# Kernel tuning notes

Hardware: AMD Instinct MI355X
Metric: run time of the kernel (lower is better)

The kernel has to match this reference:

```python
import jax, jax.numpy as jnp
import numpy as np

# ---- config constants (from ResidualNetConfig) ----
BOUND_LO = jnp.array([-5.0, -5.0, -5.0], dtype=jnp.float32)
BOUND_DIS = jnp.array([10.0, 10.0, 10.0], dtype=jnp.float32)
N_MIN = 200                 # int(ceil(max extent)/resolution) = 10/0.05
PER_LEVEL_SCALE = 2.0
NUM_LEVELS = 4
LOG2_T = 19
T = 1 << LOG2_T
OUTPUT_SDF_SCALE = 0.1
LEAKY_SLOPE = 0.01

# Instant-NGP spatial hash primes (first coord uses 1)
PRIMES = (np.uint32(1), np.uint32(2654435761), np.uint32(805459861))
# 8 corner offsets of the unit cube, [8, 3]
CORNERS = jnp.array([[(c >> d) & 1 for d in range(3)] for c in range(8)], dtype=jnp.uint32)


def hash_grid_encode(xyz01, tables):
    """xyz01: [N,3] in [0,1]; tables: [L,T,F] -> [N, L*F] trilinear hashed features."""
    feats = []
    for l in range(NUM_LEVELS):
        res = jnp.float32(N_MIN * (PER_LEVEL_SCALE ** l))
        pos = xyz01 * res                       # [N,3]
        pfloor = jnp.floor(pos)
        frac = pos - pfloor                     # [N,3]
        base = pfloor.astype(jnp.uint32)        # [N,3]
        corner = base[:, None, :] + CORNERS[None, :, :]   # [N,8,3]
        h = (corner[..., 0] * PRIMES[0]) ^ (corner[..., 1] * PRIMES[1]) ^ (corner[..., 2] * PRIMES[2])
        idx = (h & jnp.uint32(T - 1)).astype(jnp.int32)   # [N,8]
        f = tables[l][idx]                      # [N,8,F] irregular gather
        # trilinear weights: prod over dims of frac (corner=1) or 1-frac (corner=0)
        w = jnp.prod(jnp.where(CORNERS[None].astype(bool), frac[:, None, :], 1.0 - frac[:, None, :]), axis=-1)  # [N,8]
        feats.append(jnp.sum(f * w[..., None], axis=1))   # [N,F]
    return jnp.concatenate(feats, axis=-1)      # [N, L*F]


def leaky_relu(x):
    return jnp.where(x >= 0, x, LEAKY_SLOPE * x)


def setup_inputs() -> dict:
    key = jax.random.key(0)
    k1, k2, k3, k4, k5 = jax.random.split(key, 5)
    N = 2_000_000
    xyz = jax.random.uniform(k1, (N, 3), dtype=jnp.float32) * BOUND_DIS + BOUND_LO
    tables = jax.random.normal(k2, (NUM_LEVELS, T, 2), dtype=jnp.float32) * 1e-2
    W_in = jax.random.normal(k3, (8, 64), dtype=jnp.float32) / np.sqrt(8.0)
    W_h = jax.random.normal(k4, (64, 64), dtype=jnp.float32) / np.sqrt(64.0)
    W_out = jax.random.normal(k5, (64, 1), dtype=jnp.float32) / np.sqrt(64.0)
    return {"xyz": xyz, "tables": tables, "W_in": W_in, "W_h": W_h, "W_out": W_out}


def reference(xyz, tables, W_in, W_h, W_out):
    # scale_with_bound: map xyz into [0,1]^3
    xyz01 = (xyz - BOUND_LO) / BOUND_DIS
    enc = hash_grid_encode(xyz01, tables)        # [N, 8]
    h = leaky_relu(enc @ W_in)                   # hidden layer 1
    h = leaky_relu(h @ W_h)                      # hidden layer 2
    sdf = (h @ W_out).reshape(-1) * OUTPUT_SDF_SCALE
    return sdf
```

## Files before the change

kernel.cpp:

```cpp
#include <hip/hip_runtime.h>
#include <hip/hip_fp16.h>

static constexpr unsigned TSIZE = 1u << 19;
static constexpr unsigned TMASK = TSIZE - 1u;

typedef _Float16 f16;
typedef f16   f16x8 __attribute__((ext_vector_type(8)));
typedef float f32x4 __attribute__((ext_vector_type(4)));

union H2U { __half2 h; unsigned u; };

__global__ __launch_bounds__(256)
void cvt_tables(const float4* __restrict__ in, __half2* __restrict__ out, int n4)
{
    int i = blockIdx.x * 256 + threadIdx.x;
    if (i < n4) {
        float4 v = in[i];
        out[2 * i]     = __floats2half2_rn(v.x, v.y);
        out[2 * i + 1] = __floats2half2_rn(v.z, v.w);
    }
}

__device__ __forceinline__ void hash_level(float px, float py, float pz, int l,
                                           const __half2* __restrict__ tab,
                                           float& e0, float& e1)
{
    const float res = 200.0f * (float)(1 << l);
    const float fx = px * res, fy = py * res, fz = pz * res;
    const float flx = floorf(fx), fly = floorf(fy), flz = floorf(fz);
    const float frx = fx - flx, fry = fy - fly, frz = fz - flz;
    const unsigned bx = (unsigned)flx, by = (unsigned)fly, bz = (unsigned)flz;
    const unsigned hy0 = by * 2654435761u, hy1 = (by + 1u) * 2654435761u;
    const unsigned hz0 = bz * 805459861u,  hz1 = (bz + 1u) * 805459861u;
    const float wx[2] = {1.0f - frx, frx};
    const float wy[2] = {1.0f - fry, fry};
    const float wz[2] = {1.0f - frz, frz};
    e0 = 0.0f; e1 = 0.0f;
    #pragma unroll
    for (int c = 0; c < 8; ++c) {
        unsigned h = (bx + (unsigned)(c & 1))
                   ^ ((c & 2) ? hy1 : hy0)
                   ^ ((c & 4) ? hz1 : hz0);
        __half2 fv = tab[h & TMASK];
        float2 f = __half22float2(fv);
        float w = wx[c & 1] * wy[(c >> 1) & 1] * wz[(c >> 2) & 1];
        e0 = fmaf(f.x, w, e0);
        e1 = fmaf(f.y, w, e1);
    }
}

__device__ __forceinline__ void stage_xyz(const float* __restrict__ xyz, int bbase, int N,
                                          float* sxyz, float& px, float& py, float& pz)
{
    const int g3 = bbase * 3;
    #pragma unroll
    for (int t = 0; t < 3; ++t) {
        int sidx = (int)threadIdx.x + t * 256;
        int g = g3 + sidx;
        sxyz[sidx] = (g < 3 * N) ? __builtin_nontemporal_load(&xyz[g]) : 0.0f;
    }
    __syncthreads();
    px = (sxyz[threadIdx.x * 3 + 0] + 5.0f) * 0.1f;
    py = (sxyz[threadIdx.x * 3 + 1] + 5.0f) * 0.1f;
    pz = (sxyz[threadIdx.x * 3 + 2] + 5.0f) * 0.1f;
}

__global__ __launch_bounds__(256, 8)
void encode01(const float* __restrict__ xyz, const __half2* __restrict__ tab16,
              unsigned long long* __restrict__ enc01, int N)
{
    __shared__ float sxyz[768];
    const int bbase = blockIdx.x * 256;
    const int i = bbase + (int)threadIdx.x;
    float px, py, pz;
    stage_xyz(xyz, bbase, N, sxyz, px, py, pz);

    float e0, e1, e2, e3;
    hash_level(px, py, pz, 0, tab16,         e0, e1);
    hash_level(px, py, pz, 1, tab16 + TSIZE, e2, e3);

    H2U a, b;
    a.h = __floats2half2_rn(e0, e1);
    b.h = __floats2half2_rn(e2, e3);
    if (i < N) {
        unsigned long long v = (unsigned long long)a.u
                             | ((unsigned long long)b.u << 32);
        __builtin_nontemporal_store(v, &enc01[i]);
    }
}

static constexpr int H1_STRIDE = 72;

__global__ __launch_bounds__(256, 2)
void mlp23_mfma(const float* __restrict__ xyz, const __half2* __restrict__ tab16,
                const unsigned long long* __restrict__ enc01,
                const float* __restrict__ Win, const float* __restrict__ Wh,
                const float* __restrict__ Wout, float* __restrict__ out, int N)
{
    __shared__ float sxyz[768];
    __shared__ f16 h1s[256 * H1_STRIDE];

    const int bbase = blockIdx.x * 256;
    const int i = bbase + (int)threadIdx.x;
    float px, py, pz;
    stage_xyz(xyz, bbase, N, sxyz, px, py, pz);

    float enc[8];
    {
        unsigned long long v = __builtin_nontemporal_load(&enc01[i < N ? i : 0]);
        H2U a, b; a.u = (unsigned)v; b.u = (unsigned)(v >> 32);
        float2 f01 = __half22float2(a.h);
        float2 f23 = __half22float2(b.h);
        enc[0] = f01.x; enc[1] = f01.y; enc[2] = f23.x; enc[3] = f23.y;
    }
    hash_level(px, py, pz, 2, tab16 + 2 * TSIZE, enc[4], enc[5]);
    hash_level(px, py, pz, 3, tab16 + 3 * TSIZE, enc[6], enc[7]);

    float h1[64];
    #pragma unroll
    for (int j = 0; j < 64; ++j) h1[j] = 0.0f;
    #pragma unroll
    for (int k = 0; k < 8; ++k) {
        const float e = enc[k];
        #pragma unroll
        for (int j = 0; j < 64; ++j)
            h1[j] = fmaf(e, Win[k * 64 + j], h1[j]);
    }
    {
        f16* row = &h1s[(int)threadIdx.x * H1_STRIDE];
        #pragma unroll
        for (int jj = 0; jj < 8; ++jj) {
            f16x8 v;
            #pragma unroll
            for (int e = 0; e < 8; ++e) {
                float a = h1[jj * 8 + e];
                a = (a >= 0.0f) ? a : 0.01f * a;
                v[e] = (f16)a;
            }
            *(f16x8*)(row + jj * 8) = v;
        }
    }
    __syncthreads();

    const int wave = (int)threadIdx.x >> 6;
    const int lane = (int)threadIdx.x & 63;
    const int c = lane & 15;
    const int q = lane >> 4;
    const f16* wbase = &h1s[wave * 64 * H1_STRIDE];

    f16x8 bfrag[2][4];
    #pragma unroll
    for (int kt = 0; kt < 2; ++kt)
        #pragma unroll
        for (int nt = 0; nt < 4; ++nt)
            #pragma unroll
            for (int j = 0; j < 8; ++j)
                bfrag[kt][nt][j] = (f16)Wh[(kt * 32 + q * 8 + j) * 64 + nt * 16 + c];

    f32x4 Ct[4][4];
    #pragma unroll
    for (int mt = 0; mt < 4; ++mt)
        #pragma unroll
        for (int nt = 0; nt < 4; ++nt)
            Ct[mt][nt] = (f32x4){0.f, 0.f, 0.f, 0.f};

    #pragma unroll
    for (int mt = 0; mt < 4; ++mt) {
        #pragma unroll
        for (int kt = 0; kt < 2; ++kt) {
            const f16x8 a = *(const f16x8*)&wbase[(mt * 16 + c) * H1_STRIDE + kt * 32 + q * 8];
            #pragma unroll
            for (int nt = 0; nt < 4; ++nt)
                Ct[mt][nt] = __builtin_amdgcn_mfma_f32_16x16x32_f16(a, bfrag[kt][nt], Ct[mt][nt], 0, 0, 0);
        }
    }

    float acc3[4][4];
    #pragma unroll
    for (int mt = 0; mt < 4; ++mt)
        #pragma unroll
        for (int r = 0; r < 4; ++r) acc3[mt][r] = 0.0f;

    #pragma unroll
    for (int nt = 0; nt < 4; ++nt) {
        const float wo = Wout[nt * 16 + c];
        #pragma unroll
        for (int mt = 0; mt < 4; ++mt)
            #pragma unroll
            for (int r = 0; r < 4; ++r) {
                float v = Ct[mt][nt][r];
                v = (v >= 0.0f) ? v : 0.01f * v;
                acc3[mt][r] = fmaf(v, wo, acc3[mt][r]);
            }
    }
    #pragma unroll
    for (int mask = 1; mask <= 8; mask <<= 1)
        #pragma unroll
        for (int mt = 0; mt < 4; ++mt)
            #pragma unroll
            for (int r = 0; r < 4; ++r)
                acc3[mt][r] += __shfl_xor(acc3[mt][r], mask, 64);

    if (c == 0) {
        #pragma unroll
        for (int mt = 0; mt < 4; ++mt)
            #pragma unroll
            for (int r = 0; r < 4; ++r) {
                int p = bbase + wave * 64 + mt * 16 + q * 4 + r;
                if (p < N) out[p] = acc3[mt][r] * 0.1f;
            }
    }
}

__global__ __launch_bounds__(256, 2)
void resnet_mono(const float* __restrict__ xyz, const float* __restrict__ tables,
                 const float* __restrict__ Win, const float* __restrict__ Wh,
                 const float* __restrict__ Wout, float* __restrict__ out, int N)
{
    __shared__ float sxyz[768];
    const int bbase = blockIdx.x * 256;
    const int i = bbase + (int)threadIdx.x;
    float px, py, pz;
    stage_xyz(xyz, bbase, N, sxyz, px, py, pz);

    float enc[8];
    #pragma unroll
    for (int l = 0; l < 4; ++l) {
        const float res = 200.0f * (float)(1 << l);
        const float fx = px * res, fy = py * res, fz = pz * res;
        const float flx = floorf(fx), fly = floorf(fy), flz = floorf(fz);
        const float frx = fx - flx, fry = fy - fly, frz = fz - flz;
        const unsigned bx = (unsigned)flx, by = (unsigned)fly, bz = (unsigned)flz;
        const unsigned hy0 = by * 2654435761u, hy1 = (by + 1u) * 2654435761u;
        const unsigned hz0 = bz * 805459861u,  hz1 = (bz + 1u) * 805459861u;
        const float wx[2] = {1.0f - frx, frx};
        const float wy[2] = {1.0f - fry, fry};
        const float wz[2] = {1.0f - frz, frz};
        const float2* tab = (const float2*)tables + (size_t)l * TSIZE;
        float e0 = 0.0f, e1 = 0.0f;
        #pragma unroll
        for (int cc = 0; cc < 8; ++cc) {
            unsigned h = (bx + (unsigned)(cc & 1))
                       ^ ((cc & 2) ? hy1 : hy0)
                       ^ ((cc & 4) ? hz1 : hz0);
            float2 f = tab[h & TMASK];
            float w = wx[cc & 1] * wy[(cc >> 1) & 1] * wz[(cc >> 2) & 1];
            e0 = fmaf(f.x, w, e0);
            e1 = fmaf(f.y, w, e1);
        }
        enc[2 * l] = e0; enc[2 * l + 1] = e1;
    }

    float h1[64];
    #pragma unroll
    for (int j = 0; j < 64; ++j) h1[j] = 0.0f;
    #pragma unroll
    for (int k = 0; k < 8; ++k) {
        const float e = enc[k];
        #pragma unroll
        for (int j = 0; j < 64; ++j)
            h1[j] = fmaf(e, Win[k * 64 + j], h1[j]);
    }
    #pragma unroll
    for (int j = 0; j < 64; ++j)
        h1[j] = (h1[j] >= 0.0f) ? h1[j] : 0.01f * h1[j];

    float sdf = 0.0f;
    #pragma unroll
    for (int j0 = 0; j0 < 64; j0 += 16) {
        float acc[16];
        #pragma unroll
        for (int jj = 0; jj < 16; ++jj) acc[jj] = 0.0f;
        #pragma unroll
        for (int k = 0; k < 64; ++k) {
            const float hk = h1[k];
            #pragma unroll
            for (int jj = 0; jj < 16; ++jj)
                acc[jj] = fmaf(hk, Wh[k * 64 + j0 + jj], acc[jj]);
        }
        #pragma unroll
        for (int jj = 0; jj < 16; ++jj) {
            float a = acc[jj];
            a = (a >= 0.0f) ? a : 0.01f * a;
            sdf = fmaf(a, Wout[j0 + jj], sdf);
        }
    }
    if (i < N) out[i] = sdf * 0.1f;
}

extern "C" void kernel_launch(void* const* d_in, const int* in_sizes, int n_in,
                              void* d_out, int out_size, void* d_ws, size_t ws_size,
                              hipStream_t stream) {
    const float* xyz    = (const float*)d_in[0];
    const float* tables = (const float*)d_in[1];
    const float* Win    = (const float*)d_in[2];
    const float* Wh     = (const float*)d_in[3];
    const float* Wout   = (const float*)d_in[4];
    float* out = (float*)d_out;

    const int N = in_sizes[0] / 3;
    const int blocks = (N + 255) / 256;

    const int tab_floats = in_sizes[1];
    const size_t tab16_bytes = (size_t)tab_floats * 2;
    const size_t enc01_bytes = (size_t)N * 8;

    if (ws_size >= tab16_bytes + enc01_bytes) {
        __half2* tab16 = (__half2*)d_ws;
        unsigned long long* enc01 = (unsigned long long*)((char*)d_ws + tab16_bytes);
        int n4 = tab_floats / 4;
        hipLaunchKernelGGL(cvt_tables, dim3((n4 + 255) / 256), dim3(256), 0, stream,
                           (const float4*)tables, tab16, n4);
        hipLaunchKernelGGL(encode01, dim3(blocks), dim3(256), 0, stream,
                           xyz, tab16, enc01, N);
        hipLaunchKernelGGL(mlp23_mfma, dim3(blocks), dim3(256), 0, stream,
                           xyz, tab16, enc01, Win, Wh, Wout, out, N);
    } else {
        hipLaunchKernelGGL(resnet_mono, dim3(blocks), dim3(256), 0, stream,
                           xyz, tables, Win, Wh, Wout, out, N);
    }
}
```

Before: 324.9 us.

## Fuse level 0-1 encoding into MFMA MLP kernel and pre-transpose Wh to fp16

Merges the separate encode01 kernel into the main MFMA kernel, which now computes all four hash levels itself. This removes the intermediate enc01 buffer write and read and one launch, at the cost of more gather latency inside a kernel limited to 2 blocks per SM. A tiny kernel now pre-transposes and converts Wh to fp16 so each thread loads its B fragments as single vector loads instead of strided scalar float loads. The earlier split may have been chosen to give the gathers higher occupancy, which the fused kernel gives up.

```diff
diff --git a/kernel.cpp b/kernel.cpp
--- a/kernel.cpp
+++ b/kernel.cpp
@@ -7,8 +7,6 @@
 typedef _Float16 f16;
 typedef f16   f16x8 __attribute__((ext_vector_type(8)));
 typedef float f32x4 __attribute__((ext_vector_type(4)));
-
-union H2U { __half2 h; unsigned u; };
 
 __global__ __launch_bounds__(256)
 void cvt_tables(const float4* __restrict__ in, __half2* __restrict__ out, int n4)
@@ -18,6 +16,18 @@
         float4 v = in[i];
         out[2 * i]     = __floats2half2_rn(v.x, v.y);
         out[2 * i + 1] = __floats2half2_rn(v.z, v.w);
+    }
+}
+
+__global__ __launch_bounds__(256)
+void cvt_wht(const float* __restrict__ Wh, f16* __restrict__ wht)
+{
+    int t = threadIdx.x;
+    #pragma unroll
+    for (int e = 0; e < 16; ++e) {
+        int idx = t * 16 + e;
+        int n = idx >> 6, k = idx & 63;
+        wht[n * 64 + k] = (f16)Wh[k * 64 + n];
     }
 }
 
@@ -49,70 +59,37 @@
     }
 }
 
-__device__ __forceinline__ void stage_xyz(const float* __restrict__ xyz, int bbase, int N,
-                                          float* sxyz, float& px, float& py, float& pz)
-{
-    const int g3 = bbase * 3;
-    #pragma unroll
-    for (int t = 0; t < 3; ++t) {
-        int sidx = (int)threadIdx.x + t * 256;
-        int g = g3 + sidx;
-        sxyz[sidx] = (g < 3 * N) ? __builtin_nontemporal_load(&xyz[g]) : 0.0f;
-    }
-    __syncthreads();
-    px = (sxyz[threadIdx.x * 3 + 0] + 5.0f) * 0.1f;
-    py = (sxyz[threadIdx.x * 3 + 1] + 5.0f) * 0.1f;
-    pz = (sxyz[threadIdx.x * 3 + 2] + 5.0f) * 0.1f;
-}
-
-__global__ __launch_bounds__(256, 8)
-void encode01(const float* __restrict__ xyz, const __half2* __restrict__ tab16,
-              unsigned long long* __restrict__ enc01, int N)
+static constexpr int H1_STRIDE = 72;
+
+__global__ __launch_bounds__(256, 2)
+void resnet_mfma(const float* __restrict__ xyz, const __half2* __restrict__ tab16,
+                 const f16* __restrict__ wht,
+                 const float* __restrict__ Win,
+                 const float* __restrict__ Wout, float* __restrict__ out, int N)
 {
     __shared__ float sxyz[768];
+    __shared__ f16 h1s[256 * H1_STRIDE];
+
     const int bbase = blockIdx.x * 256;
     const int i = bbase + (int)threadIdx.x;
-    float px, py, pz;
-    stage_xyz(xyz, bbase, N, sxyz, px, py, pz);
-
-    float e0, e1, e2, e3;
-    hash_level(px, py, pz, 0, tab16,         e0, e1);
-    hash_level(px, py, pz, 1, tab16 + TSIZE, e2, e3);
-
-    H2U a, b;
-    a.h = __floats2half2_rn(e0, e1);
-    b.h = __floats2half2_rn(e2, e3);
-    if (i < N) {
-        unsigned long long v = (unsigned long long)a.u
-                             | ((unsigned long long)b.u << 32);
-        __builtin_nontemporal_store(v, &enc01[i]);
-    }
-}
-
-static constexpr int H1_STRIDE = 72;
-
-__global__ __launch_bounds__(256, 2)
-void mlp23_mfma(const float* __restrict__ xyz, const __half2* __restrict__ tab16,
-                const unsigned long long* __restrict__ enc01,
-                const float* __restrict__ Win, const float* __restrict__ Wh,
-                const float* __restrict__ Wout, float* __restrict__ out, int N)
-{
-    __shared__ float sxyz[768];
-    __shared__ f16 h1s[256 * H1_STRIDE];
-
-    const int bbase = blockIdx.x * 256;
-    const int i = bbase + (int)threadIdx.x;
-    float px, py, pz;
-    stage_xyz(xyz, bbase, N, sxyz, px, py, pz);
+
+    {
+        const int g3 = bbase * 3;
+        #pragma unroll
+        for (int t = 0; t < 3; ++t) {
+            int sidx = (int)threadIdx.x + t * 256;
+            int g = g3 + sidx;
+            sxyz[sidx] = (g < 3 * N) ? __builtin_nontemporal_load(&xyz[g]) : 0.0f;
+        }
+    }
+    __syncthreads();
+    const float px = (sxyz[threadIdx.x * 3 + 0] + 5.0f) * 0.1f;
+    const float py = (sxyz[threadIdx.x * 3 + 1] + 5.0f) * 0.1f;
+    const float pz = (sxyz[threadIdx.x * 3 + 2] + 5.0f) * 0.1f;
 
     float enc[8];
-    {
-        unsigned long long v = __builtin_nontemporal_load(&enc01[i < N ? i : 0]);
-        H2U a, b; a.u = (unsigned)v; b.u = (unsigned)(v >> 32);
-        float2 f01 = __half22float2(a.h);
-        float2 f23 = __half22float2(b.h);
-        enc[0] = f01.x; enc[1] = f01.y; enc[2] = f23.x; enc[3] = f23.y;
-    }
+    hash_level(px, py, pz, 0, tab16,             enc[0], enc[1]);
+    hash_level(px, py, pz, 1, tab16 + TSIZE,     enc[2], enc[3]);
     hash_level(px, py, pz, 2, tab16 + 2 * TSIZE, enc[4], enc[5]);
     hash_level(px, py, pz, 3, tab16 + 3 * TSIZE, enc[6], enc[7]);
 
@@ -153,9 +130,7 @@
     for (int kt = 0; kt < 2; ++kt)
         #pragma unroll
         for (int nt = 0; nt < 4; ++nt)
-            #pragma unroll
-            for (int j = 0; j < 8; ++j)
-                bfrag[kt][nt][j] = (f16)Wh[(kt * 32 + q * 8 + j) * 64 + nt * 16 + c];
+            bfrag[kt][nt] = *(const f16x8*)&wht[(nt * 16 + c) * 64 + kt * 32 + q * 8];
 
     f32x4 Ct[4][4];
     #pragma unroll
@@ -220,8 +195,19 @@
     __shared__ float sxyz[768];
     const int bbase = blockIdx.x * 256;
     const int i = bbase + (int)threadIdx.x;
-    float px, py, pz;
-    stage_xyz(xyz, bbase, N, sxyz, px, py, pz);
+    {
+        const int g3 = bbase * 3;
+        #pragma unroll
+        for (int t = 0; t < 3; ++t) {
+            int sidx = (int)threadIdx.x + t * 256;
+            int g = g3 + sidx;
+            sxyz[sidx] = (g < 3 * N) ? xyz[g] : 0.0f;
+        }
+    }
+    __syncthreads();
+    const float px = (sxyz[threadIdx.x * 3 + 0] + 5.0f) * 0.1f;
+    const float py = (sxyz[threadIdx.x * 3 + 1] + 5.0f) * 0.1f;
+    const float pz = (sxyz[threadIdx.x * 3 + 2] + 5.0f) * 0.1f;
 
     float enc[8];
     #pragma unroll
@@ -303,18 +289,17 @@
 
     const int tab_floats = in_sizes[1];
     const size_t tab16_bytes = (size_t)tab_floats * 2;
-    const size_t enc01_bytes = (size_t)N * 8;
-
-    if (ws_size >= tab16_bytes + enc01_bytes) {
+    const size_t wht_bytes   = 64 * 64 * sizeof(f16);
+
+    if (ws_size >= tab16_bytes + wht_bytes) {
         __half2* tab16 = (__half2*)d_ws;
-        unsigned long long* enc01 = (unsigned long long*)((char*)d_ws + tab16_bytes);
+        f16*     wht   = (f16*)((char*)d_ws + tab16_bytes);
         int n4 = tab_floats / 4;
         hipLaunchKernelGGL(cvt_tables, dim3((n4 + 255) / 256), dim3(256), 0, stream,
                            (const float4*)tables, tab16, n4);
-        hipLaunchKernelGGL(encode01, dim3(blocks), dim3(256), 0, stream,
-                           xyz, tab16, enc01, N);
-        hipLaunchKernelGGL(mlp23_mfma, dim3(blocks), dim3(256), 0, stream,
-                           xyz, tab16, enc01, Win, Wh, Wout, out, N);
+        hipLaunchKernelGGL(cvt_wht, dim3(1), dim3(256), 0, stream, Wh, wht);
+        hipLaunchKernelGGL(resnet_mfma, dim3(blocks), dim3(256), 0, stream,
+                           xyz, tab16, wht, Win, Wout, out, N);
     } else {
         hipLaunchKernelGGL(resnet_mono, dim3(blocks), dim3(256), 0, stream,
                            xyz, tables, Win, Wh, Wout, out, N);
```

Result: slower. 389.9 us (+20.0%).
